# Optimization experiments

Measured on AMD Instinct MI355X. Metric: run time of the kernel, lower is better.

Reference implementation:

```python
import jax, jax.numpy as jnp
import numpy as np

WS = 7   # window size
ES = 3   # expand size
NH = 16  # num heads

def _rel_pos_index(ws):
    coords = np.stack(np.meshgrid(np.arange(ws), np.arange(ws), indexing='ij'))
    cf = coords.reshape(2, -1)
    rel = (cf[:, :, None] - cf[:, None, :]).transpose(1, 2, 0).astype(np.int64)
    rel[..., 0] += ws - 1
    rel[..., 1] += ws - 1
    rel[..., 0] *= 2 * ws - 1
    return rel.sum(-1)  # (ws*ws, ws*ws)

def _valid_ind_rolled(ws, es):
    m_tl = np.ones((ws, ws)); m_tl[:-es, :-es] = 0
    m_tr = np.ones((ws, ws)); m_tr[:-es, es:] = 0
    m_bl = np.ones((ws, ws)); m_bl[es:, :-es] = 0
    m_br = np.ones((ws, ws)); m_br[es:, es:] = 0
    m = np.stack([m_tl, m_tr, m_bl, m_br], 0).reshape(-1)
    return np.nonzero(m)[0]  # (132,)

def _window_partition(t, ws):
    B, H, W, C = t.shape
    t = t.reshape(B, H // ws, ws, W // ws, ws, C)
    return jnp.transpose(t, (0, 1, 3, 2, 4, 5)).reshape(-1, ws * ws, C)

def setup_inputs():
    key = jax.random.key(0)
    ks = jax.random.split(key, 6)
    B, H, W, C = 8, 56, 56, 512
    n_rolled = len(_valid_ind_rolled(WS, ES))  # 132
    return {
        'x': jax.random.normal(ks[0], (B, H, W, C), jnp.float32),
        'qkv_w': jax.random.normal(ks[1], (3 * C, C), jnp.float32) * 0.02,
        'qkv_b': jnp.zeros((3 * C,), jnp.float32),
        'proj_w': jax.random.normal(ks[2], (C, C), jnp.float32) * 0.02,
        'proj_b': jnp.zeros((C,), jnp.float32),
        'rpb_table': jax.random.normal(ks[3], ((2 * WS - 1) * (2 * WS - 1), NH), jnp.float32) * 0.02,
        'rpb_neighbors': jax.random.normal(ks[4], (1, NH, WS * WS, n_rolled), jnp.float32) * 0.02,
    }

def reference(x, qkv_w, qkv_b, proj_w, proj_b, rpb_table, rpb_neighbors):
    B, H, W, C = x.shape
    hd = C // NH
    scale = hd ** -0.5
    wa = WS * WS
    qkv = x @ qkv_w.T + qkv_b  # (B,H,W,3C)
    q, k, v = jnp.split(qkv, 3, axis=-1)

    def to_win_heads(t):
        tw = _window_partition(t, WS)  # (nWB, wa, C)
        return jnp.transpose(tw.reshape(-1, wa, NH, hd), (0, 2, 1, 3))  # (nWB, NH, wa, hd)

    q_w, k_w, v_w = map(to_win_heads, (q, k, v))

    valid = jnp.asarray(_valid_ind_rolled(WS, ES))
    shifts = [(-ES, -ES), (-ES, ES), (ES, -ES), (ES, ES)]
    k_roll = jnp.concatenate([_window_partition(jnp.roll(k, s, axis=(1, 2)), WS) for s in shifts], axis=1)
    v_roll = jnp.concatenate([_window_partition(jnp.roll(v, s, axis=(1, 2)), WS) for s in shifts], axis=1)
    # (nWB, 4*wa, C) -> heads -> keep only valid rolled positions (132)
    k_roll = jnp.transpose(k_roll.reshape(-1, 4 * wa, NH, hd), (0, 2, 1, 3))[:, :, valid]
    v_roll = jnp.transpose(v_roll.reshape(-1, 4 * wa, NH, hd), (0, 2, 1, 3))[:, :, valid]

    k_all = jnp.concatenate([k_w, k_roll], axis=2)  # (nWB, NH, wa+132, hd)
    v_all = jnp.concatenate([v_w, v_roll], axis=2)

    attn = jnp.einsum('wnqd,wnkd->wnqk', q_w * scale, k_all)
    rel_idx = jnp.asarray(_rel_pos_index(WS))
    bias_win = jnp.transpose(rpb_table[rel_idx], (2, 0, 1))[None]  # (1,NH,wa,wa)
    bias = jnp.concatenate([bias_win, rpb_neighbors], axis=-1)      # (1,NH,wa,wa+132)
    attn = jax.nn.softmax(attn + bias, axis=-1)
    out = jnp.einsum('wnqk,wnkd->wnqd', attn, v_all)
    out = jnp.transpose(out, (0, 2, 1, 3)).reshape(-1, wa, C)  # (nWB, wa, C)
    return out @ proj_w.T + proj_b
```

## Files before the change

### kernel.cpp

```cpp
#include <hip/hip_runtime.h>
#include <hip/hip_bf16.h>
#include <math.h>

typedef unsigned short u16;
typedef unsigned int   u32;
typedef unsigned long long u64;
typedef __attribute__((ext_vector_type(8))) short short8;
typedef __attribute__((ext_vector_type(4))) float f32x4;

#define NHEADS 16
#define HD     32
#define WA     49
#define NROLL  132
#define NKV    181
#define NKVT   192
#define CDIM   512
#define QKVLD  1536
#define NPIX   25088
#define NWIN   512
#define VP  200
#define PSP 200
#define LOG2E 1.4426950408889634f

__device__ __forceinline__ u16 f32_to_bf16(float f) {
    union { float f; u32 u; } x; x.f = f;
    u32 r = x.u + 0x7FFFu + ((x.u >> 16) & 1u);
    return (u16)(r >> 16);
}
__device__ __forceinline__ u16 cvt_bf16_hw(float f) {
    __hip_bfloat16 h = __float2bfloat16(f);
    return *reinterpret_cast<u16*>(&h);
}

__global__ __launch_bounds__(256) void cvt3_bf16(
    const float* __restrict__ in0, u16* __restrict__ out0, int n0,
    const float* __restrict__ in1, u16* __restrict__ out1, int n1,
    const float* __restrict__ in2, u16* __restrict__ out2, int n2)
{
    int i = (blockIdx.x * 256 + threadIdx.x) * 4;
    const float* in; u16* out;
    if (i < n0)            { in = in0; out = out0; }
    else if (i < n0 + n1)  { in = in1; out = out1; i -= n0; }
    else if (i < n0 + n1 + n2) { in = in2; out = out2; i -= n0 + n1; }
    else return;
    float4 v = *(const float4*)(in + i);
    *(ushort4*)(out + i) = make_ushort4(f32_to_bf16(v.x), f32_to_bf16(v.y),
                                        f32_to_bf16(v.z), f32_to_bf16(v.w));
}

__global__ __launch_bounds__(256) void build_bias(
    const float* __restrict__ rpbt,
    const float* __restrict__ rpbn,
    float* __restrict__ bt)
{
    const int idx  = blockIdx.x * 256 + threadIdx.x;
    const int h    = idx / 12288;
    const int rem  = idx % 12288;
    const int qt   = rem / 3072;
    const int rem2 = rem % 3072;
    const int n    = rem2 / 256;
    const int rem3 = rem2 % 256;
    const int lane = rem3 / 4;
    const int r    = rem3 % 4;
    const int qi = qt * 16 + (lane & 15);
    const int kv = n * 16 + (lane >> 4) * 4 + r;
    float v = -1e30f;
    if (qi < WA && kv < NKV) {
        if (kv < WA) {
            const int r1 = qi / 7, c1 = qi % 7, r2 = kv / 7, c2 = kv % 7;
            v = rpbt[((r1 - r2 + 6) * 13 + (c1 - c2 + 6)) * NHEADS + h];
        } else {
            v = rpbn[(h * WA + qi) * NROLL + (kv - WA)];
        }
    }
    bt[idx] = v * LOG2E;
}

template<bool STORE_BF16>
__global__ __launch_bounds__(256) void gemm_mfma(
    const u16* __restrict__ A, const u16* __restrict__ W,
    const float* __restrict__ bias, void* __restrict__ Cv,
    int M, int N, int K)
{
    __shared__ __align__(16) u16 As[128 * 32];
    __shared__ __align__(16) u16 Bs[128 * 32];
    const int tid = threadIdx.x;
    const int lane = tid & 63, wv = tid >> 6;
    const int bid = blockIdx.x;
    const int nid = (bid & 7) * (gridDim.x >> 3) + (bid >> 3);
    const int nbx = N >> 7;
    const int m0 = (nid / nbx) * 128, n0 = (nid % nbx) * 128;
    const int wr = (wv >> 1) * 64, wc = (wv & 1) * 64;
    const int lr = lane & 15;
    const int lk = (lane >> 4) * 8;
    const int srow = lane >> 2;
    const int scol = (lane & 3) * 8;

    f32x4 acc[4][4] = {};

    for (int k0 = 0; k0 < K; k0 += 32) {
        __syncthreads();
        #pragma unroll
        for (int blk = 0; blk < 2; ++blk) {
            const int r = wv * 32 + blk * 16;
            __builtin_amdgcn_global_load_lds(
                (const __attribute__((address_space(1))) void*)
                    (A + (size_t)(m0 + r + srow) * K + k0 + scol),
                (__attribute__((address_space(3))) void*)(As + r * 32), 16, 0, 0);
            __builtin_amdgcn_global_load_lds(
                (const __attribute__((address_space(1))) void*)
                    (W + (size_t)(n0 + r + srow) * K + k0 + scol),
                (__attribute__((address_space(3))) void*)(Bs + r * 32), 16, 0, 0);
        }
        __syncthreads();
        #pragma unroll
        for (int mi = 0; mi < 4; ++mi) {
            const short8 af = *(const short8*)(As + (wr + mi * 16 + lr) * 32 + lk);
            #pragma unroll
            for (int ni = 0; ni < 4; ++ni) {
                const short8 bf = *(const short8*)(Bs + (wc + ni * 16 + lr) * 32 + lk);
                acc[mi][ni] = __builtin_amdgcn_mfma_f32_16x16x32_bf16(af, bf, acc[mi][ni], 0, 0, 0);
            }
        }
    }

    const int hi = lane >> 4;
    if (STORE_BF16) {
        __syncthreads();
        u16* scr = ((wv < 2) ? As : Bs) + (wv & 1) * 2048;
        u16* C = (u16*)Cv;
        #pragma unroll
        for (int mi = 0; mi < 4; ++mi) {
            #pragma unroll
            for (int ni = 0; ni < 4; ++ni) {
                const float bcol = bias[n0 + wc + ni * 16 + lr];
                #pragma unroll
                for (int r = 0; r < 4; ++r)
                    scr[(hi * 4 + r) * 68 + ni * 16 + lr] =
                        f32_to_bf16(acc[mi][ni][r] + bcol);
            }
            asm volatile("" ::: "memory");
            #pragma unroll
            for (int i = 0; i < 4; ++i) {
                const int rl = i * 4 + hi;
                const u64 v = *(const u64*)(scr + rl * 68 + (lane & 15) * 4);
                *(u64*)(C + (size_t)(m0 + wr + mi * 16 + rl) * N
                          + n0 + wc + (lane & 15) * 4) = v;
            }
            asm volatile("" ::: "memory");
        }
    } else {
        const int col0 = n0 + wc + lr;
        #pragma unroll
        for (int ni = 0; ni < 4; ++ni) {
            const float bcol = bias[col0 + ni * 16];
            #pragma unroll
            for (int mi = 0; mi < 4; ++mi)
                #pragma unroll
                for (int r = 0; r < 4; ++r) {
                    const int row = m0 + wr + mi * 16 + hi * 4 + r;
                    ((float*)Cv)[(size_t)row * N + col0 + ni * 16] = acc[mi][ni][r] + bcol;
                }
        }
    }
}

struct OffT { int dr[NROLL]; int dc[NROLL]; };
constexpr bool rvalid(int s, int r, int c) {
    return (s == 0) ? (r >= 4 || c >= 4) :
           (s == 1) ? (r >= 4 || c <= 2) :
           (s == 2) ? (r <= 2 || c >= 4) :
                      (r <= 2 || c <= 2);
}
constexpr OffT make_offt() {
    OffT t{};
    int p = 0;
    for (int s = 0; s < 4; ++s)
        for (int r = 0; r < 7; ++r)
            for (int c = 0; c < 7; ++c)
                if (rvalid(s, r, c)) {
                    const int sh = (s < 2) ? -3 : 3;
                    const int sw = (s & 1) ? 3 : -3;
                    t.dr[p] = r - sh;
                    t.dc[p] = c - sw;
                    ++p;
                }
    return t;
}
__device__ constexpr OffT OFT = make_offt();

__global__ __launch_bounds__(256, 4) void attn_win(
    const u16* __restrict__ qkvb,
    const float* __restrict__ bt,
    u16* __restrict__ aob)
{
    __shared__ __align__(16) u16 Vt[32 * VP];
    __shared__ __align__(16) u16 Ps[64 * PSP];
    __shared__ int pixt[NKV];

    const int tid  = threadIdx.x;
    const int lane = tid & 63, wv = tid >> 6;
    const int bid  = blockIdx.x;
    const int nid  = (bid & 7) * (NWIN * NHEADS / 8) + (bid >> 3);
    const int w    = nid >> 4;
    const int head = nid & 15;
    const int b    = w >> 6;
    const int h0   = ((w >> 3) & 7) * 7;
    const int w0c  = (w & 7) * 7;
    const int pixbase = b * 3136;

    if (tid < NKV) {
        int h, wc;
        if (tid < WA) { h = h0 + tid / 7; wc = w0c + tid % 7; }
        else {
            const int i = tid - WA;
            h = h0 + OFT.dr[i];  h += (h < 0) ? 56 : 0;  h -= (h >= 56) ? 56 : 0;
            wc = w0c + OFT.dc[i]; wc += (wc < 0) ? 56 : 0; wc -= (wc >= 56) ? 56 : 0;
        }
        pixt[tid] = (pixbase + h * 56 + wc) * QKVLD + head * HD;
    }
    __syncthreads();

    const int lr = lane & 15;
    const int hi = lane >> 4;
    const int lk = hi * 8;
    const int qrow0 = 16 * wv + hi * 4;

    const int qr = 16 * wv + lr;
    const short8 aq = *(const short8*)(qkvb + pixt[(qr < WA) ? qr : 0] + lk);
    short8 bk[12];
    #pragma unroll
    for (int n = 0; n < 12; ++n) {
        const int kvr = n * 16 + lr;
        bk[n] = *(const short8*)(qkvb + pixt[(kvr < NKV) ? kvr : 0] + CDIM + lk);
    }

    u64 vdat[6];
    #pragma unroll
    for (int it = 0; it < 6; ++it) {
        const int idx = tid + it * 256;
        if (idx < NKV * 8)
            vdat[it] = *(const u64*)(qkvb + pixt[idx >> 3] + 2 * CDIM + (idx & 7) * 4);
    }
    #pragma unroll
    for (int it = 0; it < 6; ++it) {
        const int idx = tid + it * 256;
        if (idx < NKV * 8) {
            const int kv = idx >> 3, dq = idx & 7;
            #pragma unroll
            for (int j = 0; j < 4; ++j)
                Vt[(dq * 4 + j) * VP + kv] = (u16)(vdat[it] >> (16 * j));
        }
    }
    for (int idx = tid; idx < 32 * (NKVT - NKV); idx += 256)
        Vt[(idx / (NKVT - NKV)) * VP + NKV + idx % (NKVT - NKV)] = 0;

    f32x4 s[12];
    __builtin_amdgcn_s_setprio(1);
    #pragma unroll
    for (int n = 0; n < 12; ++n)
        s[n] = __builtin_amdgcn_mfma_f32_16x16x32_bf16(bk[n], aq, (f32x4){0.f, 0.f, 0.f, 0.f}, 0, 0, 0);
    __builtin_amdgcn_s_setprio(0);

    const float scale2 = 0.17677669529663687f * LOG2E;
    const float* btb = bt + (((size_t)head * 4 + wv) * 12) * 256 + lane * 4;
    u16* const prow_ptr = Ps + (16 * wv + lr) * PSP + hi * 4;
    float t = 0.f;
    #pragma unroll
    for (int n = 0; n < 12; ++n) {
        const float4 b4 = *(const float4*)(btb + n * 256);
        const float e0 = exp2f(fmaf(s[n][0], scale2, b4.x));
        const float e1 = exp2f(fmaf(s[n][1], scale2, b4.y));
        const float e2 = exp2f(fmaf(s[n][2], scale2, b4.z));
        const float e3 = exp2f(fmaf(s[n][3], scale2, b4.w));
        t += (e0 + e1) + (e2 + e3);
        const u32 lo  = (u32)cvt_bf16_hw(e0) | ((u32)cvt_bf16_hw(e1) << 16);
        const u32 hi2 = (u32)cvt_bf16_hw(e2) | ((u32)cvt_bf16_hw(e3) << 16);
        *(u64*)(prow_ptr + n * 16) = (u64)lo | ((u64)hi2 << 32);
    }
    t += __shfl_xor(t, 16);
    t += __shfl_xor(t, 32);
    const float inv = 1.f / fmaxf(t, 1e-30f);
    float inv4[4];
    #pragma unroll
    for (int r = 0; r < 4; ++r)
        inv4[r] = __shfl(inv, (lane & 48) | (hi * 4 + r));

    __syncthreads();
    asm volatile("" ::: "memory");

    f32x4 o[2] = {{0.f, 0.f, 0.f, 0.f}, {0.f, 0.f, 0.f, 0.f}};
    __builtin_amdgcn_s_setprio(1);
    #pragma unroll
    for (int kk = 0; kk < 6; ++kk) {
        const short8 pa = *(const short8*)(Ps + (16 * wv + lr) * PSP + kk * 32 + lk);
        #pragma unroll
        for (int n0 = 0; n0 < 2; ++n0) {
            const short8 vb = *(const short8*)(Vt + (n0 * 16 + lr) * VP + kk * 32 + lk);
            o[n0] = __builtin_amdgcn_mfma_f32_16x16x32_bf16(pa, vb, o[n0], 0, 0, 0);
        }
    }
    __builtin_amdgcn_s_setprio(0);
    #pragma unroll
    for (int n0 = 0; n0 < 2; ++n0)
        #pragma unroll
        for (int r = 0; r < 4; ++r) {
            const int qi = qrow0 + r;
            if (qi < WA)
                aob[(size_t)(w * WA + qi) * CDIM + head * HD + n0 * 16 + lr] =
                    cvt_bf16_hw(o[n0][r] * inv4[r]);
        }
}

extern "C" void kernel_launch(void* const* d_in, const int* in_sizes, int n_in,
                              void* d_out, int out_size, void* d_ws, size_t ws_size,
                              hipStream_t stream)
{
    const float* x      = (const float*)d_in[0];
    const float* qkv_w  = (const float*)d_in[1];
    const float* qkv_b  = (const float*)d_in[2];
    const float* proj_w = (const float*)d_in[3];
    const float* proj_b = (const float*)d_in[4];
    const float* rpbt   = (const float*)d_in[5];
    const float* rpbn   = (const float*)d_in[6];

    u16* xb   = (u16*)d_ws;
    u16* qkvb = xb + (size_t)NPIX * CDIM;
    u16* aob  = qkvb + (size_t)NPIX * QKVLD;
    u16* qwb  = aob + (size_t)NPIX * CDIM;
    u16* pwb  = qwb + (size_t)QKVLD * CDIM;
    float* bt = (float*)(pwb + (size_t)CDIM * CDIM);
    const size_t need = ((size_t)NPIX * CDIM + (size_t)NPIX * QKVLD + (size_t)NPIX * CDIM
                         + (size_t)QKVLD * CDIM + (size_t)CDIM * CDIM) * sizeof(u16)
                        + (size_t)NHEADS * NKVT * 64 * sizeof(float);
    if (ws_size < need) return;

    {
        const int nx = NPIX * CDIM;
        const int nq = QKVLD * CDIM;
        const int np = CDIM * CDIM;
        const int tot4 = (nx + nq + np) / 4;
        cvt3_bf16<<<(tot4 + 255) / 256, 256, 0, stream>>>(
            x, xb, nx, qkv_w, qwb, nq, proj_w, pwb, np);
        build_bias<<<(NHEADS * NKVT * 64) / 256, 256, 0, stream>>>(rpbt, rpbn, bt);
    }

    gemm_mfma<true><<<(NPIX / 128) * (QKVLD / 128), 256, 0, stream>>>(
        xb, qwb, qkv_b, qkvb, NPIX, QKVLD, CDIM);

    attn_win<<<NWIN * NHEADS, 256, 0, stream>>>(qkvb, bt, aob);

    gemm_mfma<false><<<(NPIX / 128) * (CDIM / 128), 256, 0, stream>>>(
        aob, pwb, proj_b, d_out, NPIX, CDIM, CDIM);
}
```

Measured before the change: 194.4 us.

## Chunk attention QK/softmax/PV into streamed groups and widen GEMM K-tile

The attention kernel now processes the 192 keys in three groups of 64. For each group it computes QK scores, writes exp values into a small per-wave P buffer, and immediately accumulates the PV product, while prefetching the next group's K fragments. This shrinks the P scratch stride from 200 to 68 and cuts register use, which lets the occupancy hint rise from 4 to 5 blocks per CU. Separately, the GEMM K-tile doubles from 32 to 64, halving barrier and loop overhead per k-step at the cost of twice the LDS per block. The P buffer is reused per wave without a barrier, so correctness depends on wave-local LDS ordering.

```diff
diff --git a/kernel.cpp b/kernel.cpp
--- a/kernel.cpp
+++ b/kernel.cpp
@@ -19,7 +19,7 @@
 #define NPIX   25088
 #define NWIN   512
 #define VP  200
-#define PSP 200
+#define PSP 68
 #define LOG2E 1.4426950408889634f
 
 __device__ __forceinline__ u16 f32_to_bf16(float f) {
@@ -82,8 +82,8 @@
     const float* __restrict__ bias, void* __restrict__ Cv,
     int M, int N, int K)
 {
-    __shared__ __align__(16) u16 As[128 * 32];
-    __shared__ __align__(16) u16 Bs[128 * 32];
+    __shared__ __align__(16) u16 As[128 * 64];
+    __shared__ __align__(16) u16 Bs[128 * 64];
     const int tid = threadIdx.x;
     const int lane = tid & 63, wv = tid >> 6;
     const int bid = blockIdx.x;
@@ -93,33 +93,36 @@
     const int wr = (wv >> 1) * 64, wc = (wv & 1) * 64;
     const int lr = lane & 15;
     const int lk = (lane >> 4) * 8;
-    const int srow = lane >> 2;
-    const int scol = (lane & 3) * 8;
+    const int srow = lane >> 3;
+    const int scol = (lane & 7) * 8;
 
     f32x4 acc[4][4] = {};
 
-    for (int k0 = 0; k0 < K; k0 += 32) {
+    for (int k0 = 0; k0 < K; k0 += 64) {
         __syncthreads();
         #pragma unroll
-        for (int blk = 0; blk < 2; ++blk) {
-            const int r = wv * 32 + blk * 16;
+        for (int blk = 0; blk < 4; ++blk) {
+            const int r = wv * 32 + blk * 8;
             __builtin_amdgcn_global_load_lds(
                 (const __attribute__((address_space(1))) void*)
                     (A + (size_t)(m0 + r + srow) * K + k0 + scol),
-                (__attribute__((address_space(3))) void*)(As + r * 32), 16, 0, 0);
+                (__attribute__((address_space(3))) void*)(As + r * 64), 16, 0, 0);
             __builtin_amdgcn_global_load_lds(
                 (const __attribute__((address_space(1))) void*)
                     (W + (size_t)(n0 + r + srow) * K + k0 + scol),
-                (__attribute__((address_space(3))) void*)(Bs + r * 32), 16, 0, 0);
+                (__attribute__((address_space(3))) void*)(Bs + r * 64), 16, 0, 0);
         }
         __syncthreads();
         #pragma unroll
-        for (int mi = 0; mi < 4; ++mi) {
-            const short8 af = *(const short8*)(As + (wr + mi * 16 + lr) * 32 + lk);
-            #pragma unroll
-            for (int ni = 0; ni < 4; ++ni) {
-                const short8 bf = *(const short8*)(Bs + (wc + ni * 16 + lr) * 32 + lk);
-                acc[mi][ni] = __builtin_amdgcn_mfma_f32_16x16x32_bf16(af, bf, acc[mi][ni], 0, 0, 0);
+        for (int kk = 0; kk < 2; ++kk) {
+            #pragma unroll
+            for (int mi = 0; mi < 4; ++mi) {
+                const short8 af = *(const short8*)(As + (wr + mi * 16 + lr) * 64 + kk * 32 + lk);
+                #pragma unroll
+                for (int ni = 0; ni < 4; ++ni) {
+                    const short8 bf = *(const short8*)(Bs + (wc + ni * 16 + lr) * 64 + kk * 32 + lk);
+                    acc[mi][ni] = __builtin_amdgcn_mfma_f32_16x16x32_bf16(af, bf, acc[mi][ni], 0, 0, 0);
+                }
             }
         }
     }
@@ -189,7 +192,7 @@
 }
 __device__ constexpr OffT OFT = make_offt();
 
-__global__ __launch_bounds__(256, 4) void attn_win(
+__global__ __launch_bounds__(256, 5) void attn_win(
     const u16* __restrict__ qkvb,
     const float* __restrict__ bt,
     u16* __restrict__ aob)
@@ -228,12 +231,6 @@
 
     const int qr = 16 * wv + lr;
     const short8 aq = *(const short8*)(qkvb + pixt[(qr < WA) ? qr : 0] + lk);
-    short8 bk[12];
-    #pragma unroll
-    for (int n = 0; n < 12; ++n) {
-        const int kvr = n * 16 + lr;
-        bk[n] = *(const short8*)(qkvb + pixt[(kvr < NKV) ? kvr : 0] + CDIM + lk);
-    }
 
     u64 vdat[6];
     #pragma unroll
@@ -255,29 +252,67 @@
     for (int idx = tid; idx < 32 * (NKVT - NKV); idx += 256)
         Vt[(idx / (NKVT - NKV)) * VP + NKV + idx % (NKVT - NKV)] = 0;
 
-    f32x4 s[12];
-    __builtin_amdgcn_s_setprio(1);
-    #pragma unroll
-    for (int n = 0; n < 12; ++n)
-        s[n] = __builtin_amdgcn_mfma_f32_16x16x32_bf16(bk[n], aq, (f32x4){0.f, 0.f, 0.f, 0.f}, 0, 0, 0);
-    __builtin_amdgcn_s_setprio(0);
+    short8 bk[2][4];
+    #pragma unroll
+    for (int j = 0; j < 4; ++j) {
+        const int kvr = j * 16 + lr;
+        bk[0][j] = *(const short8*)(qkvb + pixt[(kvr < NKV) ? kvr : 0] + CDIM + lk);
+    }
+
+    __syncthreads();
 
     const float scale2 = 0.17677669529663687f * LOG2E;
     const float* btb = bt + (((size_t)head * 4 + wv) * 12) * 256 + lane * 4;
-    u16* const prow_ptr = Ps + (16 * wv + lr) * PSP + hi * 4;
+    u16* const prow_ptr = Ps + (16 * wv + lr) * PSP;
+    const u16* const parow = Ps + (16 * wv + lr) * PSP;
     float t = 0.f;
-    #pragma unroll
-    for (int n = 0; n < 12; ++n) {
-        const float4 b4 = *(const float4*)(btb + n * 256);
-        const float e0 = exp2f(fmaf(s[n][0], scale2, b4.x));
-        const float e1 = exp2f(fmaf(s[n][1], scale2, b4.y));
-        const float e2 = exp2f(fmaf(s[n][2], scale2, b4.z));
-        const float e3 = exp2f(fmaf(s[n][3], scale2, b4.w));
-        t += (e0 + e1) + (e2 + e3);
-        const u32 lo  = (u32)cvt_bf16_hw(e0) | ((u32)cvt_bf16_hw(e1) << 16);
-        const u32 hi2 = (u32)cvt_bf16_hw(e2) | ((u32)cvt_bf16_hw(e3) << 16);
-        *(u64*)(prow_ptr + n * 16) = (u64)lo | ((u64)hi2 << 32);
-    }
+    f32x4 o[2] = {{0.f, 0.f, 0.f, 0.f}, {0.f, 0.f, 0.f, 0.f}};
+
+    #pragma unroll
+    for (int g = 0; g < 3; ++g) {
+        if (g < 2) {
+            #pragma unroll
+            for (int j = 0; j < 4; ++j) {
+                const int kvr = (g + 1) * 64 / 4 * 4 + j * 16 + lr;
+                bk[(g + 1) & 1][j] =
+                    *(const short8*)(qkvb + pixt[(kvr < NKV) ? kvr : 0] + CDIM + lk);
+            }
+        }
+        f32x4 s4[4];
+        __builtin_amdgcn_s_setprio(1);
+        #pragma unroll
+        for (int j = 0; j < 4; ++j)
+            s4[j] = __builtin_amdgcn_mfma_f32_16x16x32_bf16(
+                bk[g & 1][j], aq, (f32x4){0.f, 0.f, 0.f, 0.f}, 0, 0, 0);
+        __builtin_amdgcn_s_setprio(0);
+        #pragma unroll
+        for (int j = 0; j < 4; ++j) {
+            const int n = g * 4 + j;
+            const float4 b4 = *(const float4*)(btb + n * 256);
+            const float e0 = exp2f(fmaf(s4[j][0], scale2, b4.x));
+            const float e1 = exp2f(fmaf(s4[j][1], scale2, b4.y));
+            const float e2 = exp2f(fmaf(s4[j][2], scale2, b4.z));
+            const float e3 = exp2f(fmaf(s4[j][3], scale2, b4.w));
+            t += (e0 + e1) + (e2 + e3);
+            const u32 lo  = (u32)cvt_bf16_hw(e0) | ((u32)cvt_bf16_hw(e1) << 16);
+            const u32 hi2 = (u32)cvt_bf16_hw(e2) | ((u32)cvt_bf16_hw(e3) << 16);
+            *(u64*)(prow_ptr + j * 16 + hi * 4) = (u64)lo | ((u64)hi2 << 32);
+        }
+        asm volatile("" ::: "memory");
+        __builtin_amdgcn_s_setprio(1);
+        #pragma unroll
+        for (int kkl = 0; kkl < 2; ++kkl) {
+            const short8 pa = *(const short8*)(parow + kkl * 32 + lk);
+            #pragma unroll
+            for (int n0 = 0; n0 < 2; ++n0) {
+                const short8 vb = *(const short8*)(Vt + (n0 * 16 + lr) * VP + (g * 2 + kkl) * 32 + lk);
+                o[n0] = __builtin_amdgcn_mfma_f32_16x16x32_bf16(pa, vb, o[n0], 0, 0, 0);
+            }
+        }
+        __builtin_amdgcn_s_setprio(0);
+        asm volatile("" ::: "memory");
+    }
+
     t += __shfl_xor(t, 16);
     t += __shfl_xor(t, 32);
     const float inv = 1.f / fmaxf(t, 1e-30f);
@@ -286,21 +321,6 @@
     for (int r = 0; r < 4; ++r)
         inv4[r] = __shfl(inv, (lane & 48) | (hi * 4 + r));
 
-    __syncthreads();
-    asm volatile("" ::: "memory");
-
-    f32x4 o[2] = {{0.f, 0.f, 0.f, 0.f}, {0.f, 0.f, 0.f, 0.f}};
-    __builtin_amdgcn_s_setprio(1);
-    #pragma unroll
-    for (int kk = 0; kk < 6; ++kk) {
-        const short8 pa = *(const short8*)(Ps + (16 * wv + lr) * PSP + kk * 32 + lk);
-        #pragma unroll
-        for (int n0 = 0; n0 < 2; ++n0) {
-            const short8 vb = *(const short8*)(Vt + (n0 * 16 + lr) * VP + kk * 32 + lk);
-            o[n0] = __builtin_amdgcn_mfma_f32_16x16x32_bf16(pa, vb, o[n0], 0, 0, 0);
-        }
-    }
-    __builtin_amdgcn_s_setprio(0);
     #pragma unroll
     for (int n0 = 0; n0 < 2; ++n0)
         #pragma unroll
```

After: 193.5 us. About the same (-0.5%).
